# Kernel tuning notes

Hardware: AMD Instinct MI355X
Metric: run time of the kernel (lower is better)

## Reference

```python
import jax, jax.numpy as jnp
import numpy as np

B, N, D, E = 2, 50000, 128, 640000


def setup_inputs() -> dict:
    key = jax.random.key(0)
    ks = jax.random.split(key, 7)
    x = jax.random.normal(ks[0], (B, N, D), dtype=jnp.float32)
    edge_index = jax.random.randint(ks[1], (2, E), 0, N)
    edge_attr = jax.random.uniform(ks[2], (E,), dtype=jnp.float32)
    s = 1.0 / np.sqrt(D)
    W1 = jax.random.uniform(ks[3], (D, D), jnp.float32, -s, s)
    b1 = jax.random.uniform(ks[4], (D,), jnp.float32, -s, s)
    W2 = jax.random.uniform(ks[5], (D, D), jnp.float32, -s, s)
    b2 = jax.random.uniform(ks[6], (D,), jnp.float32, -s, s)
    return {"x": x, "edge_index": edge_index, "edge_attr": edge_attr,
            "W1": W1, "b1": b1, "W2": W2, "b2": b2}


def _gcn_layer(x, W, b, row, col, norm, n):
    # x: [B, N, D] -> transform then gather-scale-scatter along edges
    h = jnp.einsum('bnd,df->bnf', x, W)
    msg = h[:, row, :] * norm[None, :, None]          # [B, E2, D]
    agg = jax.vmap(lambda m: jax.ops.segment_sum(m, col, num_segments=n))(msg)
    return agg + b


def reference(x, edge_index, edge_attr, W1, b1, W2, b2):
    n = x.shape[1]
    row, col = edge_index[0], edge_index[1]
    # GCNConv default: add self loops (weight 1), symmetric normalization
    loop = jnp.arange(n)
    row2 = jnp.concatenate([row, loop])
    col2 = jnp.concatenate([col, loop])
    w2 = jnp.concatenate([edge_attr, jnp.ones((n,), edge_attr.dtype)])
    deg = jax.ops.segment_sum(w2, col2, num_segments=n)
    dinv = jnp.where(deg > 0, jax.lax.rsqrt(deg), 0.0)
    norm = dinv[row2] * w2 * dinv[col2]               # [E2]
    # dropout is identity in eval mode
    h = jax.nn.relu(_gcn_layer(x, W1, b1, row2, col2, norm, n))
    h = jax.nn.relu(_gcn_layer(h, W2, b2, row2, col2, norm, n))
    return h
```

## Files before the change

kernel.cpp:

```cpp
#include <hip/hip_runtime.h>

#define NNODES 50000
#define NBATCH 2
#define DIM    128
#define NEDGE  640000
#define M_TOT  (NBATCH*NNODES)
#define NXCD   8
#define NBL_N  196

typedef unsigned short u16;
typedef unsigned int   u32;
typedef unsigned long long u64;

typedef __attribute__((ext_vector_type(8))) short bf16x8;
typedef __attribute__((ext_vector_type(4))) float f32x4;

__device__ __forceinline__ float bf2f(u16 u){ return __uint_as_float(((u32)u)<<16); }
__device__ __forceinline__ u16 f2bf(float f){
    u32 x = __float_as_uint(f);
    x += 0x7fffu + ((x>>16)&1u);
    return (u16)(x>>16);
}

__global__ __launch_bounds__(256) void count_k(const int* __restrict__ ei,
                                               const float* __restrict__ ea,
                                               u64* __restrict__ part,
                                               u32* __restrict__ rankpack){
    u32 xcc = __builtin_amdgcn_s_getreg(6164) & 7u;
    int e = blockIdx.x*256 + threadIdx.x;
    if (e < NEDGE){
        int c = ei[NEDGE + e];
        u64 inc = (((u64)__float2uint_rn(ea[e] * 16777216.0f)) << 32) | 1ull;
        u64 old = __hip_atomic_fetch_add(&part[(size_t)xcc*NNODES + c], inc,
                                         __ATOMIC_RELAXED, __HIP_MEMORY_SCOPE_WORKGROUP);
        rankpack[e] = ((u32)old & 0xffffu) | (xcc << 16);
    }
}

__global__ __launch_bounds__(256) void scan1(const u64* __restrict__ part,
                                             int* __restrict__ cnt,
                                             int* __restrict__ poff,
                                             float* __restrict__ dinv,
                                             int* colstart, int* bsum){
    __shared__ int s[256];
    int tid = threadIdx.x;
    int n = blockIdx.x*256 + tid;
    int v = 0;
    if (n < NNODES){
        int run = 0; u64 fsum = 0;
        #pragma unroll
        for (int p = 0; p < NXCD; ++p){
            u64 pv = part[(size_t)p*NNODES + n];
            poff[p*NNODES + n] = run;
            run  += (int)(pv & 0xffffffffu);
            fsum += (pv >> 32);
        }
        cnt[n] = run;
        v = run;
        float deg = 1.0f + (float)fsum * (1.0f/16777216.0f);
        dinv[n] = rsqrtf(deg);
    }
    s[tid] = v; __syncthreads();
    #pragma unroll
    for (int off = 1; off < 256; off <<= 1){
        int t = (tid >= off) ? s[tid-off] : 0;
        __syncthreads();
        s[tid] += t;
        __syncthreads();
    }
    if (n < NNODES) colstart[n] = s[tid] - v;
    if (tid == 255) bsum[blockIdx.x] = s[255];
}

__global__ __launch_bounds__(256) void fill_k(const int* __restrict__ ei,
                                              const float* __restrict__ ea,
                                              const float* __restrict__ dinv,
                                              const int* __restrict__ colstart,
                                              const int* __restrict__ bsum,
                                              const int* __restrict__ poff,
                                              const u32* __restrict__ rankpack,
                                              int* __restrict__ colstartF,
                                              u32* __restrict__ epk){
    __shared__ int s[256];
    __shared__ int pre[256];
    int tid = threadIdx.x;
    int v = (tid < NBL_N) ? bsum[tid] : 0;
    s[tid] = v; __syncthreads();
    #pragma unroll
    for (int off = 1; off < 256; off <<= 1){
        int t = (tid >= off) ? s[tid-off] : 0;
        __syncthreads();
        s[tid] += t;
        __syncthreads();
    }
    pre[tid] = s[tid] - v;
    __syncthreads();

    int e = blockIdx.x*256 + tid;
    if (e < NEDGE){
        int r = ei[e], c = ei[NEDGE + e];
        u32 rp = rankpack[e];
        int base = colstart[c] + pre[c >> 8];
        colstartF[c] = base;
        int pos = base + poff[(rp >> 16)*NNODES + c] + (int)(rp & 0xffffu);
        float w = dinv[r] * ea[e] * dinv[c];
        epk[pos] = (u32)r | ((u32)f2bf(w) << 16);
    }
}

__global__ __launch_bounds__(256) void transposeW(const float* __restrict__ W1, u16* __restrict__ Wt1,
                                                  const float* __restrict__ W2, u16* __restrict__ Wt2){
    int i = blockIdx.x*256 + threadIdx.x;
    const float* W = (i < 16384) ? W1 : W2;
    u16* Wt       = (i < 16384) ? Wt1 : Wt2;
    int ii = i & 16383;
    int k = ii >> 7, n = ii & 127;
    Wt[n*DIM + k] = f2bf(W[ii]);
}

__device__ __forceinline__ bf16x8 load_frag(const float* A, size_t off){
    const float4* ap = (const float4*)(A + off);
    float4 lo = ap[0], hi = ap[1];
    bf16x8 r;
    r[0] = (short)f2bf(lo.x); r[1] = (short)f2bf(lo.y);
    r[2] = (short)f2bf(lo.z); r[3] = (short)f2bf(lo.w);
    r[4] = (short)f2bf(hi.x); r[5] = (short)f2bf(hi.y);
    r[6] = (short)f2bf(hi.z); r[7] = (short)f2bf(hi.w);
    return r;
}
__device__ __forceinline__ bf16x8 load_frag(const u16* A, size_t off){
    return *(const bf16x8*)(A + off);
}

template <typename AT>
__global__ __launch_bounds__(256) void gemm128(const AT* __restrict__ A,
                                               const u16* __restrict__ Wt,
                                               u16* __restrict__ H, int M){
    __shared__ u16 Wl[128][136];
    int tid = threadIdx.x;
    {
        const uint4* src = (const uint4*)Wt;
        #pragma unroll
        for (int j = 0; j < 8; ++j){
            int g = tid + j*256;
            int n = g >> 4;
            int k = (g & 15) * 8;
            *(uint4*)&Wl[n][k] = src[g];
        }
    }
    __syncthreads();

    int wave = tid >> 6, lane = tid & 63;
    int quad = lane >> 4, r = lane & 15;
    int row0 = blockIdx.x*256 + wave*64;

    f32x4 acc[4][8];
    #pragma unroll
    for (int mt = 0; mt < 4; ++mt)
        #pragma unroll
        for (int nt = 0; nt < 8; ++nt)
            acc[mt][nt] = (f32x4){0.f,0.f,0.f,0.f};

    #pragma unroll
    for (int ks = 0; ks < 4; ++ks){
        bf16x8 af[4];
        #pragma unroll
        for (int mt = 0; mt < 4; ++mt){
            int row = row0 + mt*16 + r;
            if (row < M)
                af[mt] = load_frag(A, (size_t)row*DIM + ks*32 + quad*8);
            else
                af[mt] = (bf16x8){0,0,0,0,0,0,0,0};
        }
        #pragma unroll
        for (int nt = 0; nt < 8; ++nt){
            bf16x8 bfr = *(const bf16x8*)&Wl[nt*16 + r][ks*32 + quad*8];
            #pragma unroll
            for (int mt = 0; mt < 4; ++mt)
                acc[mt][nt] = __builtin_amdgcn_mfma_f32_16x16x32_bf16(af[mt], bfr, acc[mt][nt], 0, 0, 0);
        }
    }

    #pragma unroll
    for (int mt = 0; mt < 4; ++mt){
        #pragma unroll
        for (int reg = 0; reg < 4; ++reg){
            int row = row0 + mt*16 + quad*4 + reg;
            if (row < M){
                #pragma unroll
                for (int nt = 0; nt < 8; ++nt)
                    H[(size_t)row*DIM + nt*16 + r] = f2bf(acc[mt][nt][reg]);
            }
        }
    }
}

template <bool OUT_F32>
__global__ __launch_bounds__(256) void gather5_k(const u16* __restrict__ H,
                                                 const u32* __restrict__ epk,
                                                 const int* __restrict__ colstartF,
                                                 const int* __restrict__ cnt,
                                                 const float* __restrict__ dinv,
                                                 const float* __restrict__ bias,
                                                 void* __restrict__ out){
    int wave = threadIdx.x >> 6, lane = threadIdx.x & 63;
    int batch = blockIdx.x & 1;
    int n = (blockIdx.x >> 1)*4 + wave;
    if (n >= NNODES) return;
    const char* Hb = (const char*)H + (size_t)batch*NNODES*256;
    int half = lane >> 5;
    int sub  = lane & 31;

    float a0, a1, a2, a3;
    {
        uint2 sv = *(const uint2*)(Hb + (size_t)n*256 + sub*8);
        float dn = dinv[n];
        float dn2 = half ? 0.f : dn*dn;
        a0 = dn2*__uint_as_float(sv.x << 16);
        a1 = dn2*__uint_as_float(sv.x & 0xffff0000u);
        a2 = dn2*__uint_as_float(sv.y << 16);
        a3 = dn2*__uint_as_float(sv.y & 0xffff0000u);
    }

    int s = colstartF[n], c = cnt[n];
    for (int base = 0; base < c; base += 64){
        int m = min(64, c - base);
        u32 em = 0;
        if (lane < m) em = epk[s + base + lane];
        for (int j = 0; j < m; j += 16){
            #pragma unroll
            for (int g = 0; g < 8; ++g){
                u32 me = __shfl(em, j + 2*g + half);
                uint2 v = *(const uint2*)(Hb + (size_t)(me & 0xffffu)*256 + sub*8);
                float w = __uint_as_float(me & 0xffff0000u);
                a0 = fmaf(w, __uint_as_float(v.x << 16), a0);
                a1 = fmaf(w, __uint_as_float(v.x & 0xffff0000u), a1);
                a2 = fmaf(w, __uint_as_float(v.y << 16), a2);
                a3 = fmaf(w, __uint_as_float(v.y & 0xffff0000u), a3);
            }
        }
    }

    a0 += __shfl_xor(a0, 32);
    a1 += __shfl_xor(a1, 32);
    a2 += __shfl_xor(a2, 32);
    a3 += __shfl_xor(a3, 32);

    if (lane < 32){
        float4 bb = ((const float4*)bias)[sub];
        a0 = fmaxf(a0 + bb.x, 0.f);
        a1 = fmaxf(a1 + bb.y, 0.f);
        a2 = fmaxf(a2 + bb.z, 0.f);
        a3 = fmaxf(a3 + bb.w, 0.f);
        if (OUT_F32){
            float* O = (float*)out + (size_t)(batch*NNODES + n)*DIM;
            *(float4*)(O + sub*4) = make_float4(a0, a1, a2, a3);
        } else {
            char* O = (char*)out + (size_t)(batch*NNODES + n)*256;
            uint2 pk;
            pk.x = (u32)f2bf(a0) | ((u32)f2bf(a1) << 16);
            pk.y = (u32)f2bf(a2) | ((u32)f2bf(a3) << 16);
            *(uint2*)(O + sub*8) = pk;
        }
    }
}

extern "C" void kernel_launch(void* const* d_in, const int* in_sizes, int n_in,
                              void* d_out, int out_size, void* d_ws, size_t ws_size,
                              hipStream_t stream){
    const float* x  = (const float*)d_in[0];
    const int*   ei = (const int*)  d_in[1];
    const float* ea = (const float*)d_in[2];
    const float* W1 = (const float*)d_in[3];
    const float* b1 = (const float*)d_in[4];
    const float* W2 = (const float*)d_in[5];
    const float* b2 = (const float*)d_in[6];

    char* p = (char*)d_ws;
    auto alloc = [&](size_t bytes)->char*{ char* r = p; p += (bytes + 511) & ~(size_t)511; return r; };
    u64*   part     = (u64*)  alloc((size_t)NXCD*NNODES*8);
    u32*   rankpack = (u32*)  alloc((size_t)NEDGE*4);
    int*   poff     = (int*)  alloc((size_t)NXCD*NNODES*4);
    float* dinv     = (float*)alloc(NNODES*4);
    int*   cnt      = (int*)  alloc(NNODES*4);
    int*   colstart = (int*)  alloc(NNODES*4);
    int*   colstartF= (int*)  alloc(NNODES*4);
    int*   bsum     = (int*)  alloc(1024);
    u32*   epk      = (u32*)  alloc((size_t)NEDGE*4);
    u16*   Wt1      = (u16*)  alloc(DIM*DIM*2);
    u16*   Wt2      = (u16*)  alloc(DIM*DIM*2);
    u16*   h        = (u16*)  alloc((size_t)M_TOT*DIM*2);
    u16*   o1       = (u16*)  alloc((size_t)M_TOT*DIM*2);

    const int NBL_E = (NEDGE  + 255)/256;
    const int NTILE = (M_TOT + 255)/256;
    const int NBL_G = 2*((NNODES + 3)/4);

    hipMemsetAsync(part, 0, (size_t)NXCD*NNODES*8, stream);
    transposeW<<<128, 256, 0, stream>>>(W1, Wt1, W2, Wt2);
    count_k<<<NBL_E, 256, 0, stream>>>(ei, ea, part, rankpack);
    scan1  <<<NBL_N, 256, 0, stream>>>(part, cnt, poff, dinv, colstart, bsum);
    fill_k <<<NBL_E, 256, 0, stream>>>(ei, ea, dinv, colstart, bsum, poff, rankpack, colstartF, epk);

    gemm128<float><<<NTILE, 256, 0, stream>>>(x, Wt1, h, M_TOT);
    gather5_k<false><<<NBL_G, 256, 0, stream>>>(h, epk, colstartF, cnt, dinv, b1, o1);
    gemm128<u16>  <<<NTILE, 256, 0, stream>>>(o1, Wt2, h, M_TOT);
    gather5_k<true> <<<NBL_G, 256, 0, stream>>>(h, epk, colstartF, cnt, dinv, b2, d_out);
}
```

Before: 284.8 us.

## Interleave batches in hidden features so one wave gathers both batches per node

The first GEMM now writes its output with the two batches interleaved per node (row 2n+b), so each node's features for both batches sit in one contiguous 512-byte row. The gather kernel then handles both batches with a single wave per node, reading each edge's metadata and doing each shuffle once, and issuing 512-byte contiguous neighbour reads instead of two 256-byte ones. The second GEMM works directly on the interleaved layout, and only the final gather converts back to the batch-major output. Separately, zeroing of the partition counters moves from a memset into the weight-transpose kernel, saving one launch.

```diff
diff --git a/kernel.cpp b/kernel.cpp
--- a/kernel.cpp
+++ b/kernel.cpp
@@ -109,13 +109,15 @@
 }
 
 __global__ __launch_bounds__(256) void transposeW(const float* __restrict__ W1, u16* __restrict__ Wt1,
-                                                  const float* __restrict__ W2, u16* __restrict__ Wt2){
+                                                  const float* __restrict__ W2, u16* __restrict__ Wt2,
+                                                  u64* __restrict__ part){
     int i = blockIdx.x*256 + threadIdx.x;
     const float* W = (i < 16384) ? W1 : W2;
     u16* Wt       = (i < 16384) ? Wt1 : Wt2;
     int ii = i & 16383;
     int k = ii >> 7, n = ii & 127;
     Wt[n*DIM + k] = f2bf(W[ii]);
+    for (int z = i; z < NXCD*NNODES; z += 32768) part[z] = 0;
 }
 
 __device__ __forceinline__ bf16x8 load_frag(const float* A, size_t off){
@@ -132,7 +134,7 @@
     return *(const bf16x8*)(A + off);
 }
 
-template <typename AT>
+template <typename AT, bool PERM>
 __global__ __launch_bounds__(256) void gemm128(const AT* __restrict__ A,
                                                const u16* __restrict__ Wt,
                                                u16* __restrict__ H, int M){
@@ -187,16 +189,24 @@
         for (int reg = 0; reg < 4; ++reg){
             int row = row0 + mt*16 + quad*4 + reg;
             if (row < M){
+                size_t hrow;
+                if (PERM){
+                    int b = (row >= NNODES);
+                    int n = row - b*NNODES;
+                    hrow = (size_t)(2*n + b);
+                } else {
+                    hrow = (size_t)row;
+                }
                 #pragma unroll
                 for (int nt = 0; nt < 8; ++nt)
-                    H[(size_t)row*DIM + nt*16 + r] = f2bf(acc[mt][nt][reg]);
+                    H[hrow*DIM + nt*16 + r] = f2bf(acc[mt][nt][reg]);
             }
         }
     }
 }
 
 template <bool OUT_F32>
-__global__ __launch_bounds__(256) void gather5_k(const u16* __restrict__ H,
+__global__ __launch_bounds__(256) void gather6_k(const u16* __restrict__ Hi,
                                                  const u32* __restrict__ epk,
                                                  const int* __restrict__ colstartF,
                                                  const int* __restrict__ cnt,
@@ -204,18 +214,14 @@
                                                  const float* __restrict__ bias,
                                                  void* __restrict__ out){
     int wave = threadIdx.x >> 6, lane = threadIdx.x & 63;
-    int batch = blockIdx.x & 1;
-    int n = (blockIdx.x >> 1)*4 + wave;
+    int n = blockIdx.x*4 + wave;
     if (n >= NNODES) return;
-    const char* Hb = (const char*)H + (size_t)batch*NNODES*256;
-    int half = lane >> 5;
-    int sub  = lane & 31;
+    const char* Hb = (const char*)Hi;
 
     float a0, a1, a2, a3;
     {
-        uint2 sv = *(const uint2*)(Hb + (size_t)n*256 + sub*8);
-        float dn = dinv[n];
-        float dn2 = half ? 0.f : dn*dn;
+        uint2 sv = *(const uint2*)(Hb + (size_t)n*512 + lane*8);
+        float dn = dinv[n], dn2 = dn*dn;
         a0 = dn2*__uint_as_float(sv.x << 16);
         a1 = dn2*__uint_as_float(sv.x & 0xffff0000u);
         a2 = dn2*__uint_as_float(sv.y << 16);
@@ -227,11 +233,11 @@
         int m = min(64, c - base);
         u32 em = 0;
         if (lane < m) em = epk[s + base + lane];
-        for (int j = 0; j < m; j += 16){
+        for (int j = 0; j < m; j += 8){
             #pragma unroll
             for (int g = 0; g < 8; ++g){
-                u32 me = __shfl(em, j + 2*g + half);
-                uint2 v = *(const uint2*)(Hb + (size_t)(me & 0xffffu)*256 + sub*8);
+                u32 me = __shfl(em, j + g);
+                uint2 v = *(const uint2*)(Hb + (size_t)(me & 0xffffu)*512 + lane*8);
                 float w = __uint_as_float(me & 0xffff0000u);
                 a0 = fmaf(w, __uint_as_float(v.x << 16), a0);
                 a1 = fmaf(w, __uint_as_float(v.x & 0xffff0000u), a1);
@@ -241,27 +247,21 @@
         }
     }
 
-    a0 += __shfl_xor(a0, 32);
-    a1 += __shfl_xor(a1, 32);
-    a2 += __shfl_xor(a2, 32);
-    a3 += __shfl_xor(a3, 32);
-
-    if (lane < 32){
-        float4 bb = ((const float4*)bias)[sub];
-        a0 = fmaxf(a0 + bb.x, 0.f);
-        a1 = fmaxf(a1 + bb.y, 0.f);
-        a2 = fmaxf(a2 + bb.z, 0.f);
-        a3 = fmaxf(a3 + bb.w, 0.f);
-        if (OUT_F32){
-            float* O = (float*)out + (size_t)(batch*NNODES + n)*DIM;
-            *(float4*)(O + sub*4) = make_float4(a0, a1, a2, a3);
-        } else {
-            char* O = (char*)out + (size_t)(batch*NNODES + n)*256;
-            uint2 pk;
-            pk.x = (u32)f2bf(a0) | ((u32)f2bf(a1) << 16);
-            pk.y = (u32)f2bf(a2) | ((u32)f2bf(a3) << 16);
-            *(uint2*)(O + sub*8) = pk;
-        }
+    int sub = lane & 31, b = lane >> 5;
+    float4 bb = ((const float4*)bias)[sub];
+    a0 = fmaxf(a0 + bb.x, 0.f);
+    a1 = fmaxf(a1 + bb.y, 0.f);
+    a2 = fmaxf(a2 + bb.z, 0.f);
+    a3 = fmaxf(a3 + bb.w, 0.f);
+    if (OUT_F32){
+        float* O = (float*)out + ((size_t)b*NNODES + n)*DIM + sub*4;
+        *(float4*)O = make_float4(a0, a1, a2, a3);
+    } else {
+        char* O = (char*)out + (size_t)n*512 + lane*8;
+        uint2 pk;
+        pk.x = (u32)f2bf(a0) | ((u32)f2bf(a1) << 16);
+        pk.y = (u32)f2bf(a2) | ((u32)f2bf(a3) << 16);
+        *(uint2*)O = pk;
     }
 }
 
@@ -294,16 +294,15 @@
 
     const int NBL_E = (NEDGE  + 255)/256;
     const int NTILE = (M_TOT + 255)/256;
-    const int NBL_G = 2*((NNODES + 3)/4);
-
-    hipMemsetAsync(part, 0, (size_t)NXCD*NNODES*8, stream);
-    transposeW<<<128, 256, 0, stream>>>(W1, Wt1, W2, Wt2);
+    const int NBL_G = (NNODES + 3)/4;
+
+    transposeW<<<128, 256, 0, stream>>>(W1, Wt1, W2, Wt2, part);
     count_k<<<NBL_E, 256, 0, stream>>>(ei, ea, part, rankpack);
     scan1  <<<NBL_N, 256, 0, stream>>>(part, cnt, poff, dinv, colstart, bsum);
     fill_k <<<NBL_E, 256, 0, stream>>>(ei, ea, dinv, colstart, bsum, poff, rankpack, colstartF, epk);
 
-    gemm128<float><<<NTILE, 256, 0, stream>>>(x, Wt1, h, M_TOT);
-    gather5_k<false><<<NBL_G, 256, 0, stream>>>(h, epk, colstartF, cnt, dinv, b1, o1);
-    gemm128<u16>  <<<NTILE, 256, 0, stream>>>(o1, Wt2, h, M_TOT);
-    gather5_k<true> <<<NBL_G, 256, 0, stream>>>(h, epk, colstartF, cnt, dinv, b2, d_out);
-}
+    gemm128<float, true ><<<NTILE, 256, 0, stream>>>(x,  Wt1, h, M_TOT);
+    gather6_k<false><<<NBL_G, 256, 0, stream>>>(h,  epk, colstartF, cnt, dinv, b1, o1);
+    gemm128<u16,   false><<<NTILE, 256, 0, stream>>>(o1, Wt2, h, M_TOT);
+    gather6_k<true ><<<NBL_G, 256, 0, stream>>>(h,  epk, colstartF, cnt, dinv, b2, d_out);
+}
```

New measurement: 283.5 us. Within noise of the previous version (-0.5%).
